# Kernel optimization log

Hardware: AMD Instinct MI355X
Metric: run time of the kernel (lower is better)

The kernel has to match this reference:

```python
import jax, jax.numpy as jnp
import numpy as np

N_NODES = 20000
N_EDGES = 640000
NUM_COUNTS = 64
NUM_FEATS = 128


def setup_inputs() -> dict:
    key = jax.random.key(0)
    k1, k2, k3, k4, k5 = jax.random.split(key, 5)
    cnt = jax.random.uniform(k1, (N_EDGES, NUM_COUNTS), dtype=jnp.float32)
    embedding = jax.random.normal(k2, (N_NODES, NUM_FEATS), dtype=jnp.float32)
    importance = jax.random.normal(k3, (NUM_COUNTS, NUM_FEATS), dtype=jnp.float32)
    src = jax.random.randint(k4, (N_EDGES,), 0, N_NODES, dtype=jnp.int32)
    # ensure every node has >=1 incoming edge so the normalization divide is well-defined
    dst = jax.random.permutation(k5, jnp.arange(N_EDGES, dtype=jnp.int32) % N_NODES)
    return {"cnt": cnt, "embedding": embedding, "importance": importance, "src": src, "dst": dst}


def reference(cnt, embedding, importance, src, dst):
    # weight = softmax over the num_counts axis (dim=0)
    weight = jax.nn.softmax(importance, axis=0)            # [C, F]
    edge_score = cnt @ weight                               # [E, F] dense GEMM
    msgs = embedding[src] * edge_score                      # [E, F] u_mul_e
    new_embedding = jax.ops.segment_sum(msgs, dst, num_segments=N_NODES)      # [N, F]
    node_score = jax.ops.segment_sum(edge_score, dst, num_segments=N_NODES)   # [N, F]
    return new_embedding / node_score
```

## Files before the change

kernel.cpp:

```cpp
#include <hip/hip_runtime.h>
#include <hip/hip_bf16.h>
#include <stdint.h>

#define NN 20000
#define NE 640000
#define NC 64
#define NF 128
#define CAP 32
#define NPW 5
#define WPB 4
#define NSTEP (2 * NPW)

typedef __attribute__((ext_vector_type(8))) short short8;
typedef __attribute__((ext_vector_type(8))) __bf16 bf16x8;
typedef __attribute__((ext_vector_type(2))) __bf16 bf16x2;
typedef __attribute__((ext_vector_type(4))) float floatx4;
typedef __attribute__((ext_vector_type(4))) unsigned int uintx4;

static __device__ __forceinline__ unsigned short f2bf(float f) {
  union { float f; unsigned int i; } v; v.f = f;
  unsigned int x = v.i;
  x += 0x7fffu + ((x >> 16) & 1u);
  return (unsigned short)(x >> 16);
}

static __device__ __forceinline__ unsigned int pk2(float a, float b) {
#if __has_builtin(__builtin_amdgcn_cvt_pk_bf16_f32)
  bf16x2 r = __builtin_amdgcn_cvt_pk_bf16_f32(a, b);
  return __builtin_bit_cast(unsigned int, r);
#else
  return (unsigned int)f2bf(a) | ((unsigned int)f2bf(b) << 16);
#endif
}

static __device__ __forceinline__ short8 cvt8(floatx4 lo, floatx4 hi) {
  uintx4 u;
  u.x = pk2(lo[0], lo[1]); u.y = pk2(lo[2], lo[3]);
  u.z = pk2(hi[0], hi[1]); u.w = pk2(hi[2], hi[3]);
  return __builtin_bit_cast(short8, u);
}

static __device__ __forceinline__ float frcp(float x) {
#if __has_builtin(__builtin_amdgcn_rcpf)
  return __builtin_amdgcn_rcpf(x);
#else
  return 1.0f / x;
#endif
}

#define GLOAD_LDS(gp, lp)                                                      \
  __builtin_amdgcn_global_load_lds(                                           \
      (const __attribute__((address_space(1))) void*)(gp),                     \
      (__attribute__((address_space(3))) void*)(lp), 16, 0, 0)

__global__ void softpack_kernel(const float* __restrict__ imp,
                                unsigned short* __restrict__ wpack) {
  __shared__ float w_s[NC][NF];
  int f = threadIdx.x;
  float v[NC];
  float mx = -1e30f;
#pragma unroll
  for (int c = 0; c < NC; ++c) { v[c] = imp[c * NF + f]; mx = fmaxf(mx, v[c]); }
  float s = 0.f;
#pragma unroll
  for (int c = 0; c < NC; ++c) { v[c] = __expf(v[c] - mx); s += v[c]; }
  float inv = 1.0f / s;
#pragma unroll
  for (int c = 0; c < NC; ++c) w_s[c][f] = v[c] * inv;
  __syncthreads();
#pragma unroll
  for (int idx = 0; idx < 8192; idx += 128) {
    int i2 = idx + f;
    int j  = i2 & 7;
    int l  = (i2 >> 3) & 63;
    int ks = (i2 >> 9) & 1;
    int nt = i2 >> 10;
    int k = ks * 32 + (l >> 4) * 8 + j;
    int n = nt * 16 + (l & 15);
    wpack[i2] = f2bf(w_s[k][n]);
  }
}

__global__ void bin_kernel(const int* __restrict__ dst,
                           int* __restrict__ counts,
                           int* __restrict__ elist,
                           int cstride) {
  int e = blockIdx.x * 256 + threadIdx.x;
  if (e < NE) {
    int n = dst[e];
    int slot = atomicAdd(&counts[(size_t)n * cstride], 1);
    if (slot < CAP) elist[n * CAP + slot] = e;
  }
}

__global__ __launch_bounds__(256) void node_kernel(
    const float* __restrict__ cnt,
    const float* __restrict__ emb,
    const int* __restrict__ srcp,
    const int* __restrict__ elist,
    const unsigned short* __restrict__ wpack,
    float* __restrict__ out)
{
  __shared__ float cnt_s[WPB][2][16 * NC];

  const int tid = threadIdx.x;
  const int wid = tid >> 6;
  const int lane = tid & 63;
  const int m = lane & 15;
  const int q = lane >> 4;
  const int base = (blockIdx.x * WPB + wid) * NPW;

  short8 wf[8][2];
#pragma unroll
  for (int nt = 0; nt < 8; ++nt)
#pragma unroll
    for (int ks = 0; ks < 2; ++ks)
      wf[nt][ks] = *(const short8*)(wpack + ((nt * 2 + ks) * 64 + lane) * 8);

  int e_cur = elist[(size_t)base * CAP + (lane & 31)];
  int s_cur = srcp[e_cur];
  int pe = 0, ps = 0;

#pragma unroll
  for (int j = 0; j < 4; ++j) {
    int rl = 4 * j + q;
    int eid = __shfl(e_cur, rl);
    int cs = m ^ (rl & 7);
    GLOAD_LDS(cnt + (size_t)eid * NC + cs * 4, &cnt_s[wid][0][j * 256]);
  }

  float ea[8], sa[8];

#pragma unroll
  for (int s = 0; s < NSTEP; ++s) {
    const int h = s & 1;
    const int node = base + (s >> 1);
    const int cbuf = s & 1;
    const bool more = (s + 1 < NSTEP);

    if (h == 0) {
#pragma unroll
      for (int t = 0; t < 8; ++t) { ea[t] = 0.f; sa[t] = 0.f; }
      if (s + 2 < NSTEP) pe = elist[(size_t)(node + 1) * CAP + (lane & 31)];
    } else if (more) {
      ps = srcp[pe];
    }

    if (more) {
#pragma unroll
      for (int j = 0; j < 4; ++j) {
        int rl = 4 * j + q;
        int eid = __shfl(h ? pe : e_cur, (h ? 0 : 16) + rl);
        int cs = m ^ (rl & 7);
        GLOAD_LDS(cnt + (size_t)eid * NC + cs * 4,
                  &cnt_s[wid][cbuf ^ 1][j * 256]);
      }
      asm volatile("s_waitcnt vmcnt(4)" ::: "memory");
    } else {
      asm volatile("s_waitcnt vmcnt(0)" ::: "memory");
    }

    const float* cb = cnt_s[wid][cbuf];
    const int sw = m & 7;
    const int rb = m * NC;
    floatx4 c0 = *(const floatx4*)&cb[rb + ((2 * q)     ^ sw) * 4];
    floatx4 c1 = *(const floatx4*)&cb[rb + ((2 * q + 1) ^ sw) * 4];
    floatx4 c2 = *(const floatx4*)&cb[rb + ((8 + 2 * q) ^ sw) * 4];
    floatx4 c3 = *(const floatx4*)&cb[rb + ((9 + 2 * q) ^ sw) * 4];
    short8 a0 = cvt8(c0, c1);
    short8 a1 = cvt8(c2, c3);

    floatx4 acc[8];
#pragma unroll
    for (int nt = 0; nt < 8; ++nt) {
#pragma unroll
      for (int r = 0; r < 4; ++r) acc[nt][r] = 0.f;
      acc[nt] = __builtin_amdgcn_mfma_f32_16x16x32_bf16(
          __builtin_bit_cast(bf16x8, a0), __builtin_bit_cast(bf16x8, wf[nt][0]),
          acc[nt], 0, 0, 0);
      acc[nt] = __builtin_amdgcn_mfma_f32_16x16x32_bf16(
          __builtin_bit_cast(bf16x8, a1), __builtin_bit_cast(bf16x8, wf[nt][1]),
          acc[nt], 0, 0, 0);
    }

#pragma unroll
    for (int nt = 0; nt < 8; ++nt)
#pragma unroll
      for (int r = 0; r < 4; ++r) sa[nt] += acc[nt][r];

#pragma unroll
    for (int r = 0; r < 4; ++r) {
      int sv = __shfl(s_cur, h * 16 + 4 * q + r);
      const float* er = emb + (size_t)sv * NF + m;
#pragma unroll
      for (int nt = 0; nt < 8; ++nt)
        ea[nt] = fmaf(acc[nt][r], er[nt * 16], ea[nt]);
    }

    if (h == 1) {
#pragma unroll
      for (int t = 0; t < 8; ++t) {
        ea[t] += __shfl_xor(ea[t], 16, 64);
        ea[t] += __shfl_xor(ea[t], 32, 64);
        sa[t] += __shfl_xor(sa[t], 16, 64);
        sa[t] += __shfl_xor(sa[t], 32, 64);
      }
      float e0 = (q & 2) ? ((q & 1) ? ea[6] : ea[4]) : ((q & 1) ? ea[2] : ea[0]);
      float e1 = (q & 2) ? ((q & 1) ? ea[7] : ea[5]) : ((q & 1) ? ea[3] : ea[1]);
      float d0 = (q & 2) ? ((q & 1) ? sa[6] : sa[4]) : ((q & 1) ? sa[2] : sa[0]);
      float d1 = (q & 2) ? ((q & 1) ? sa[7] : sa[5]) : ((q & 1) ? sa[3] : sa[1]);
      float* op = out + (size_t)node * NF;
      op[(2 * q) * 16 + m]     = e0 * frcp(d0);
      op[(2 * q + 1) * 16 + m] = e1 * frcp(d1);
      if (more) { e_cur = pe; s_cur = ps; }
    }
  }
}

extern "C" void kernel_launch(void* const* d_in, const int* in_sizes, int n_in,
                              void* d_out, int out_size, void* d_ws, size_t ws_size,
                              hipStream_t stream) {
  const float* cnt = (const float*)d_in[0];
  const float* emb = (const float*)d_in[1];
  const float* imp = (const float*)d_in[2];
  const int* src = (const int*)d_in[3];
  const int* dst = (const int*)d_in[4];
  float* out = (float*)d_out;

  char* ws = (char*)d_ws;
  unsigned short* wpack = (unsigned short*)(ws);

  const size_t need_padded = 16384 + (size_t)NN * 32 + (size_t)NN * CAP * 4;
  int cstride;
  int* counts;
  int* elist;
  if (ws_size >= need_padded) {
    cstride = 8;
    counts = (int*)(ws + 16384);
    elist  = (int*)(ws + 16384 + (size_t)NN * 32);
  } else {
    cstride = 1;
    counts = (int*)(ws + 16384);
    elist  = (int*)(ws + 98304);
  }

  hipMemsetAsync(counts, 0, (size_t)NN * cstride * sizeof(int), stream);
  softpack_kernel<<<1, NF, 0, stream>>>(imp, wpack);
  bin_kernel<<<(NE + 255) / 256, 256, 0, stream>>>(dst, counts, elist, cstride);
  node_kernel<<<NN / (WPB * NPW), 256, 0, stream>>>(cnt, emb, src, elist, wpack, out);
}
```

Before: 300.5 us.

## Fuse memset, softmax pack, binning and node pass into one cooperative kernel

Replaces the memset plus three kernel launches with a single cooperative persistent kernel. Phases are separated by grid-wide syncs, and the node work is spread over a grid capped at 1000 blocks with a task loop. The goal is to remove launch gaps and per-kernel tail effects. The cost is two grid barriers and less parallelism in the binning and node phases than the original full-size grids. If the cooperative launch fails, the code falls back to the old path.

```diff
diff --git a/kernel.cpp b/kernel.cpp
--- a/kernel.cpp
+++ b/kernel.cpp
@@ -1,6 +1,9 @@
 #include <hip/hip_runtime.h>
+#include <hip/hip_cooperative_groups.h>
 #include <hip/hip_bf16.h>
 #include <stdint.h>
+
+namespace cg = cooperative_groups;
 
 #define NN 20000
 #define NE 640000
@@ -10,6 +13,7 @@
 #define NPW 5
 #define WPB 4
 #define NSTEP (2 * NPW)
+#define NTASK (NN / NPW)
 
 typedef __attribute__((ext_vector_type(8))) short short8;
 typedef __attribute__((ext_vector_type(8))) __bf16 bf16x8;
@@ -52,6 +56,180 @@
   __builtin_amdgcn_global_load_lds(                                           \
       (const __attribute__((address_space(1))) void*)(gp),                     \
       (__attribute__((address_space(3))) void*)(lp), 16, 0, 0)
+
+__global__ __launch_bounds__(256) void fused_kernel(
+    const float* __restrict__ cnt,
+    const float* __restrict__ emb,
+    const float* __restrict__ imp,
+    const int* __restrict__ srcp,
+    const int* __restrict__ dstp,
+    int* __restrict__ counts,
+    int* __restrict__ elist,
+    unsigned short* __restrict__ wpack,
+    float* __restrict__ out,
+    int cstride)
+{
+  __shared__ float smem[WPB * 2 * 16 * NC];
+
+  const int tid = threadIdx.x;
+  const int bid = blockIdx.x;
+  const int nthr = gridDim.x * 256;
+  const int gtid = bid * 256 + tid;
+
+  for (int i = gtid; i < NN * cstride; i += nthr) counts[i] = 0;
+
+  if (bid == 0) {
+    float (*w_s)[NF] = (float(*)[NF])smem;
+    if (tid < NF) {
+      float v[NC];
+      float mx = -1e30f;
+#pragma unroll
+      for (int c = 0; c < NC; ++c) { v[c] = imp[c * NF + tid]; mx = fmaxf(mx, v[c]); }
+      float ssum = 0.f;
+#pragma unroll
+      for (int c = 0; c < NC; ++c) { v[c] = __expf(v[c] - mx); ssum += v[c]; }
+      float inv = 1.0f / ssum;
+#pragma unroll
+      for (int c = 0; c < NC; ++c) w_s[c][tid] = v[c] * inv;
+    }
+    __syncthreads();
+    for (int i2 = tid; i2 < NC * NF; i2 += 256) {
+      int j  = i2 & 7;
+      int l  = (i2 >> 3) & 63;
+      int ks = (i2 >> 9) & 1;
+      int nt = i2 >> 10;
+      int k = ks * 32 + (l >> 4) * 8 + j;
+      int n = nt * 16 + (l & 15);
+      wpack[i2] = f2bf(w_s[k][n]);
+    }
+  }
+  __threadfence();
+  cg::this_grid().sync();
+
+  for (int e = gtid; e < NE; e += nthr) {
+    int n = dstp[e];
+    int slot = atomicAdd(&counts[(size_t)n * cstride], 1);
+    if (slot < CAP) elist[n * CAP + slot] = e;
+  }
+  __threadfence();
+  cg::this_grid().sync();
+  __threadfence();
+
+  const int wid = tid >> 6;
+  const int lane = tid & 63;
+  const int m = lane & 15;
+  const int q = lane >> 4;
+  float* cbuf0 = smem + wid * (2 * 16 * NC);
+
+  short8 wf[8][2];
+#pragma unroll
+  for (int nt = 0; nt < 8; ++nt)
+#pragma unroll
+    for (int ks = 0; ks < 2; ++ks)
+      wf[nt][ks] = *(const short8*)(wpack + ((nt * 2 + ks) * 64 + lane) * 8);
+
+  for (int task = bid * WPB + wid; task < NTASK; task += gridDim.x * WPB) {
+    const int base = task * NPW;
+    int e_cur = elist[(size_t)base * CAP + (lane & 31)];
+    int s_cur = srcp[e_cur];
+    int pe = 0, ps = 0;
+
+#pragma unroll
+    for (int j = 0; j < 4; ++j) {
+      int rl = 4 * j + q;
+      int eid = __shfl(e_cur, rl);
+      int cs = m ^ (rl & 7);
+      GLOAD_LDS(cnt + (size_t)eid * NC + cs * 4, cbuf0 + j * 256);
+    }
+
+    float ea[8], sa[8];
+
+#pragma unroll
+    for (int s = 0; s < NSTEP; ++s) {
+      const int h = s & 1;
+      const int node = base + (s >> 1);
+      const int cbuf = s & 1;
+      const bool more = (s + 1 < NSTEP);
+
+      if (h == 0) {
+#pragma unroll
+        for (int t = 0; t < 8; ++t) { ea[t] = 0.f; sa[t] = 0.f; }
+        if (s + 2 < NSTEP) pe = elist[(size_t)(node + 1) * CAP + (lane & 31)];
+      } else if (more) {
+        ps = srcp[pe];
+      }
+
+      if (more) {
+#pragma unroll
+        for (int j = 0; j < 4; ++j) {
+          int rl = 4 * j + q;
+          int eid = __shfl(h ? pe : e_cur, (h ? 0 : 16) + rl);
+          int cs = m ^ (rl & 7);
+          GLOAD_LDS(cnt + (size_t)eid * NC + cs * 4,
+                    cbuf0 + (cbuf ^ 1) * 1024 + j * 256);
+        }
+        asm volatile("s_waitcnt vmcnt(4)" ::: "memory");
+      } else {
+        asm volatile("s_waitcnt vmcnt(0)" ::: "memory");
+      }
+
+      const float* cb = cbuf0 + cbuf * 1024;
+      const int sw = m & 7;
+      const int rb = m * NC;
+      floatx4 c0 = *(const floatx4*)&cb[rb + ((2 * q)     ^ sw) * 4];
+      floatx4 c1 = *(const floatx4*)&cb[rb + ((2 * q + 1) ^ sw) * 4];
+      floatx4 c2 = *(const floatx4*)&cb[rb + ((8 + 2 * q) ^ sw) * 4];
+      floatx4 c3 = *(const floatx4*)&cb[rb + ((9 + 2 * q) ^ sw) * 4];
+      short8 a0 = cvt8(c0, c1);
+      short8 a1 = cvt8(c2, c3);
+
+      floatx4 acc[8];
+#pragma unroll
+      for (int nt = 0; nt < 8; ++nt) {
+#pragma unroll
+        for (int r = 0; r < 4; ++r) acc[nt][r] = 0.f;
+        acc[nt] = __builtin_amdgcn_mfma_f32_16x16x32_bf16(
+            __builtin_bit_cast(bf16x8, a0), __builtin_bit_cast(bf16x8, wf[nt][0]),
+            acc[nt], 0, 0, 0);
+        acc[nt] = __builtin_amdgcn_mfma_f32_16x16x32_bf16(
+            __builtin_bit_cast(bf16x8, a1), __builtin_bit_cast(bf16x8, wf[nt][1]),
+            acc[nt], 0, 0, 0);
+      }
+
+#pragma unroll
+      for (int nt = 0; nt < 8; ++nt)
+#pragma unroll
+        for (int r = 0; r < 4; ++r) sa[nt] += acc[nt][r];
+
+#pragma unroll
+      for (int r = 0; r < 4; ++r) {
+        int sv = __shfl(s_cur, h * 16 + 4 * q + r);
+        const float* er = emb + (size_t)sv * NF + m;
+#pragma unroll
+        for (int nt = 0; nt < 8; ++nt)
+          ea[nt] = fmaf(acc[nt][r], er[nt * 16], ea[nt]);
+      }
+
+      if (h == 1) {
+#pragma unroll
+        for (int t = 0; t < 8; ++t) {
+          ea[t] += __shfl_xor(ea[t], 16, 64);
+          ea[t] += __shfl_xor(ea[t], 32, 64);
+          sa[t] += __shfl_xor(sa[t], 16, 64);
+          sa[t] += __shfl_xor(sa[t], 32, 64);
+        }
+        float e0 = (q & 2) ? ((q & 1) ? ea[6] : ea[4]) : ((q & 1) ? ea[2] : ea[0]);
+        float e1 = (q & 2) ? ((q & 1) ? ea[7] : ea[5]) : ((q & 1) ? ea[3] : ea[1]);
+        float d0 = (q & 2) ? ((q & 1) ? sa[6] : sa[4]) : ((q & 1) ? sa[2] : sa[0]);
+        float d1 = (q & 2) ? ((q & 1) ? sa[7] : sa[5]) : ((q & 1) ? sa[3] : sa[1]);
+        float* op = out + (size_t)node * NF;
+        op[(2 * q) * 16 + m]     = e0 * frcp(d0);
+        op[(2 * q + 1) * 16 + m] = e1 * frcp(d1);
+        if (more) { e_cur = pe; s_cur = ps; }
+      }
+    }
+  }
+}
 
 __global__ void softpack_kernel(const float* __restrict__ imp,
                                 unsigned short* __restrict__ wpack) {
@@ -94,15 +272,10 @@
 }
 
 __global__ __launch_bounds__(256) void node_kernel(
-    const float* __restrict__ cnt,
-    const float* __restrict__ emb,
-    const int* __restrict__ srcp,
-    const int* __restrict__ elist,
-    const unsigned short* __restrict__ wpack,
-    float* __restrict__ out)
-{
+    const float* __restrict__ cnt, const float* __restrict__ emb,
+    const int* __restrict__ srcp, const int* __restrict__ elist,
+    const unsigned short* __restrict__ wpack, float* __restrict__ out) {
   __shared__ float cnt_s[WPB][2][16 * NC];
-
   const int tid = threadIdx.x;
   const int wid = tid >> 6;
   const int lane = tid & 63;
@@ -244,8 +417,31 @@
     elist  = (int*)(ws + 98304);
   }
 
-  hipMemsetAsync(counts, 0, (size_t)NN * cstride * sizeof(int), stream);
-  softpack_kernel<<<1, NF, 0, stream>>>(imp, wpack);
-  bin_kernel<<<(NE + 255) / 256, 256, 0, stream>>>(dst, counts, elist, cstride);
-  node_kernel<<<NN / (WPB * NPW), 256, 0, stream>>>(cnt, emb, src, elist, wpack, out);
-}
+  static int g_grid = 0;
+  if (g_grid == 0) {
+    int nb = 0;
+    if (hipOccupancyMaxActiveBlocksPerMultiprocessor(&nb, fused_kernel, 256, 0) != hipSuccess || nb < 1)
+      nb = 2;
+    int ncu = 256;
+    int dev = 0;
+    hipDeviceProp_t prop;
+    if (hipGetDevice(&dev) == hipSuccess && hipGetDeviceProperties(&prop, dev) == hipSuccess)
+      ncu = prop.multiProcessorCount;
+    long cap = (long)nb * (long)ncu;
+    g_grid = (cap < 1000) ? (int)cap : 1000;
+    if (g_grid < 1) g_grid = 1;
+  }
+
+  void* args[] = {(void*)&cnt, (void*)&emb, (void*)&imp, (void*)&src, (void*)&dst,
+                  (void*)&counts, (void*)&elist, (void*)&wpack, (void*)&out,
+                  (void*)&cstride};
+  hipError_t ce = hipLaunchCooperativeKernel(
+      reinterpret_cast<void*>(fused_kernel), dim3(g_grid), dim3(256), args, 0, stream);
+
+  if (ce != hipSuccess) {
+    hipMemsetAsync(counts, 0, (size_t)NN * cstride * sizeof(int), stream);
+    softpack_kernel<<<1, NF, 0, stream>>>(imp, wpack);
+    bin_kernel<<<(NE + 255) / 256, 256, 0, stream>>>(dst, counts, elist, cstride);
+    node_kernel<<<NN / (WPB * NPW), 256, 0, stream>>>(cnt, emb, src, elist, wpack, out);
+  }
+}
```

Result: slower. 454.0 us (+51.1%).
